# Kernel tuning notes

Hardware: AMD Instinct MI355X
Metric: run time of the kernel (lower is better)

The kernel has to match this reference:

```python
import jax, jax.numpy as jnp
import numpy as np
from jax import lax

B, C, OUT, K, L = 8, 256, 256, 7, 2048
STRIDE, PAD, DIL = 1, 3, 1

def setup_inputs() -> dict:
    key = jax.random.key(0)
    k1, k2, k3, k4, k5 = jax.random.split(key, 5)
    return {
        "x": jax.random.normal(k1, (B, C, L), jnp.float32),
        "w_off": jax.random.normal(k2, (C * K * 2, C, K), jnp.float32) * 0.02,
        "b_off": jax.random.normal(k3, (C * K * 2,), jnp.float32) * 0.02,
        "weight": jax.random.normal(k4, (OUT, C, K), jnp.float32) * 0.02,
        "bias": jax.random.normal(k5, (OUT,), jnp.float32) * 0.02,
    }

def _gather_lin(x, idx):
    # x: (B,C,Lin), idx: (B,C,K,Lout) -> zero-padded gather along length
    Lin = x.shape[-1]
    valid = (idx >= 0) & (idx < Lin)
    idxc = jnp.clip(idx, 0, Lin - 1)
    v = jnp.take_along_axis(x[:, :, None, :], idxc, axis=3)
    return jnp.where(valid, v, jnp.zeros((), x.dtype))

def reference(x, w_off, b_off, weight, bias):
    # offset/mask predictor conv (same geometry as main conv)
    off = lax.conv_general_dilated(
        x, w_off, window_strides=(STRIDE,), padding=[(PAD, PAD)],
        rhs_dilation=(DIL,), dimension_numbers=("NCH", "OIH", "NCH"))
    off = off + b_off[None, :, None]
    Lout = off.shape[-1]
    off = off.reshape(B, 2, C * K, Lout)
    offset = off[:, 0].reshape(B, C, K, Lout)          # fractional shift per (c,k,p)
    mask = jax.nn.sigmoid(off[:, 1]).reshape(B, C, K, Lout)
    # base sampling grid: p*stride - pad + k*dil
    base = (jnp.arange(Lout) * STRIDE - PAD)[None, :] + (jnp.arange(K) * DIL)[:, None]  # (K,Lout)
    pos = offset + base[None, None].astype(x.dtype)    # (B,C,K,Lout)
    p0 = jnp.floor(pos)
    frac = pos - p0
    p0i = p0.astype(jnp.int32)
    sampled = _gather_lin(x, p0i) * (1.0 - frac) + _gather_lin(x, p0i + 1) * frac
    sampled = sampled * mask
    # grouped conv accumulate (groups=1): (B,C,K,L) x (O,C,K) -> (B,O,L)
    out = jnp.einsum("bckl,ock->bol", sampled, weight) + bias[None, :, None]
    return out
```

## Files before the change

### kernel.cpp

```cpp
#include <hip/hip_runtime.h>

typedef unsigned short ushort_t;
typedef __attribute__((ext_vector_type(8))) short bf16x8;
typedef __attribute__((ext_vector_type(4))) float f32x4;

constexpr int BB   = 8;
constexpr int CC   = 256;
constexpr int OUTC = 256;
constexpr int KK   = 7;
constexpr int LL   = 2048;
constexpr int PADc = 3;
constexpr int KD   = CC * KK;
constexpr int MOFF = CC * KK * 2;
constexpr int NTOT = BB * LL;
constexpr int NKSTEPS = KD / 32;
constexpr int LP   = LL + 6;

__device__ __forceinline__ ushort_t f2bf(float f) {
    unsigned u = __float_as_uint(f);
    unsigned r = (u + 0x7fffu + ((u >> 16) & 1u)) >> 16;
    return (ushort_t)r;
}

__global__ __launch_bounds__(256) void cast_k(const float4* __restrict__ src,
                                              ushort_t* __restrict__ dst, int n4) {
    int i = blockIdx.x * 256 + threadIdx.x;
    if (i >= n4) return;
    float4 v = src[i];
    ushort4 o;
    o.x = f2bf(v.x); o.y = f2bf(v.y); o.z = f2bf(v.z); o.w = f2bf(v.w);
    *(ushort4*)(dst + (size_t)i * 4) = o;
}

__global__ __launch_bounds__(256) void castperm_woff(const float* __restrict__ src,
                                                     ushort_t* __restrict__ dst) {
    int i = blockIdx.x * 256 + threadIdx.x;
    if (i >= MOFF * KD) return;
    int dr  = i / KD;
    int rem = i - dr * KD;
    int kk = rem >> 8, c = rem & 255;
    int r = (dr & 1) ? (KD + (dr >> 1)) : (dr >> 1);
    dst[i] = f2bf(src[(r * 256 + c) * 7 + kk]);
}

__global__ __launch_bounds__(256) void xpose_k(const float* __restrict__ x,
                                               ushort_t* __restrict__ xp) {
    __shared__ float tile[32][257];
    int bid = blockIdx.x;
    int b  = bid >> 6;
    int l0 = ((bid >> 3) & 7) * 256;
    int c0 = (bid & 7) * 32;
    int tid = threadIdx.x;
    const float* xb = x + (size_t)b * (CC * LL);
    ushort_t* xpb = xp + (size_t)b * (LP * 256);
#pragma unroll 4
    for (int k = 0; k < 32; ++k)
        tile[k][tid] = xb[(size_t)(c0 + k) * LL + l0 + tid];
    __syncthreads();
    int lp = l0 + tid + 3;
#pragma unroll
    for (int q = 0; q < 8; ++q) {
        ushort4 v;
        v.x = f2bf(tile[4 * q + 0][tid]);
        v.y = f2bf(tile[4 * q + 1][tid]);
        v.z = f2bf(tile[4 * q + 2][tid]);
        v.w = f2bf(tile[4 * q + 3][tid]);
        *(ushort4*)(xpb + (size_t)lp * 256 + c0 + 4 * q) = v;
    }
    if ((bid & 63) == 0) {
#pragma unroll
        for (int r = 0; r < 6; ++r) {
            int glp = (r < 3) ? r : (2048 + r);
            xpb[glp * 256 + tid] = 0;
        }
    }
}

__device__ __forceinline__ void load_lds16(const ushort_t* g, ushort_t* l) {
    __builtin_amdgcn_global_load_lds(
        (const __attribute__((address_space(1))) unsigned int*)g,
        (__attribute__((address_space(3))) unsigned int*)l, 16, 0, 0);
}

__device__ __forceinline__ void stage256A(ushort_t* ldsbuf,
                                          const ushort_t* __restrict__ A,
                                          int m0, int kt, int wid, int lane) {
    int t = wid * 64 + lane;
    int g = (t & 3) ^ ((t >> 3) & 3);
#pragma unroll
    for (int j = 0; j < 2; ++j) {
        int row = j * 128 + (t >> 2);
        load_lds16(A + (size_t)(m0 + row) * KD + kt * 32 + g * 8,
                   ldsbuf + j * 4096 + wid * 512);
    }
}
__device__ __forceinline__ void stage256B(ushort_t* ldsbuf,
                                          const ushort_t* __restrict__ xp,
                                          int n0, int kt, int wid, int lane) {
    int t = wid * 64 + lane;
    int g = (t & 3) ^ ((t >> 3) & 3);
    int tap = kt >> 3, cs = kt & 7;
    const ushort_t* base = xp + (size_t)(n0 >> 11) * (LP * 256)
                              + (size_t)((n0 & 2047) + tap) * 256 + cs * 32 + g * 8;
#pragma unroll
    for (int j = 0; j < 2; ++j) {
        int row = j * 128 + (t >> 2);
        load_lds16(base + (size_t)row * 256,
                   ldsbuf + 8192 + j * 4096 + wid * 512);
    }
}

template <int VMC>
__device__ __forceinline__ void kstep256(const ushort_t* __restrict__ A,
                                         const ushort_t* __restrict__ xp,
                                         ushort_t* lds, int m0, int n0, int kt,
                                         int wid, int lane, int wr, int wc,
                                         int r15, int u, f32x4 (&acc)[8][4]) {
    asm volatile("s_waitcnt vmcnt(%0)" :: "n"(VMC) : "memory");
    __builtin_amdgcn_s_barrier();
    const ushort_t* buf = lds + (size_t)(kt & 3) * 16384;
    const ushort_t* pa = buf + (wr * 128 + r15) * 32 + u * 8;
    const ushort_t* pb = buf + 8192 + (wc * 64 + r15) * 32 + u * 8;
    bf16x8 af[8], bq[4];
#pragma unroll
    for (int i = 0; i < 8; ++i) af[i] = *(const bf16x8*)(pa + i * 512);
#pragma unroll
    for (int j = 0; j < 4; ++j) bq[j] = *(const bf16x8*)(pb + j * 512);
    if (kt + 3 < NKSTEPS) {
        stage256A(lds + (size_t)((kt + 3) & 3) * 16384, A,  m0, kt + 3, wid, lane);
        stage256B(lds + (size_t)((kt + 3) & 3) * 16384, xp, n0, kt + 3, wid, lane);
    }
    __builtin_amdgcn_s_setprio(1);
#pragma unroll
    for (int i = 0; i < 8; ++i)
#pragma unroll
        for (int j = 0; j < 4; ++j)
            acc[i][j] = __builtin_amdgcn_mfma_f32_16x16x32_bf16(af[i], bq[j], acc[i][j], 0, 0, 0);
    __builtin_amdgcn_s_setprio(0);
}

__global__ __launch_bounds__(512, 2) void gemm256_off_fused(const ushort_t* __restrict__ A,
                                                            const ushort_t* __restrict__ xp,
                                                            const float* __restrict__ boff,
                                                            const float* __restrict__ x,
                                                            ushort_t* __restrict__ s) {
    __shared__ __align__(16) ushort_t lds[4 * 16384];
    constexpr int NT = NTOT / 256;
    constexpr int NWG = (MOFF / 256) * NT;
    int bid = blockIdx.x;
    int wg = (bid & 7) * (NWG / 8) + (bid >> 3);
    int mt = wg / NT, nt = wg % NT;
    int m0 = mt * 256, n0 = nt * 256;
    int tid = threadIdx.x, wid = tid >> 6, lane = tid & 63;
    int wr = wid >> 2, wc = wid & 3;
    int r15 = lane & 15, kh = lane >> 4;
    int u = kh ^ ((r15 >> 1) & 3);

    f32x4 acc[8][4] = {};

    stage256A(lds,             A,  m0, 0, wid, lane);
    stage256B(lds,             xp, n0, 0, wid, lane);
    stage256A(lds + 16384,     A,  m0, 1, wid, lane);
    stage256B(lds + 16384,     xp, n0, 1, wid, lane);
    stage256A(lds + 2 * 16384, A,  m0, 2, wid, lane);
    stage256B(lds + 2 * 16384, xp, n0, 2, wid, lane);

    for (int kt = 0; kt < NKSTEPS - 2; ++kt)
        kstep256<8>(A, xp, lds, m0, n0, kt, wid, lane, wr, wc, r15, u, acc);
    kstep256<4>(A, xp, lds, m0, n0, NKSTEPS - 2, wid, lane, wr, wc, r15, u, acc);
    kstep256<0>(A, xp, lds, m0, n0, NKSTEPS - 1, wid, lane, wr, wc, r15, u, acc);

    __syncthreads();
    ushort_t* st = lds;
#pragma unroll
    for (int i = 0; i < 8; ++i) {
        int mloc = wr * 128 + i * 16 + kh * 4;
        int ckb  = (m0 + mloc) >> 1;
        int ckl  = mloc >> 1;
        float bo0 = boff[ckb],     bm0 = boff[KD + ckb];
        float bo1 = boff[ckb + 1], bm1 = boff[KD + ckb + 1];
        int c0 = ckb / 7,       kk0 = ckb - c0 * 7;
        int c1 = (ckb + 1) / 7, kk1 = (ckb + 1) - c1 * 7;
#pragma unroll
        for (int j = 0; j < 4; ++j) {
            int nl = wc * 64 + j * 16 + r15;
            int n = n0 + nl;
            int b = n >> 11, l = n & 2047;
            const float* xb_ = x + (size_t)b * (CC * LL);
            f32x4 v = acc[i][j];
            ushort2 o2;
#pragma unroll
            for (int p = 0; p < 2; ++p) {
                float offv = v[2 * p]     + (p ? bo1 : bo0);
                float mpre = v[2 * p + 1] + (p ? bm1 : bm0);
                int c = p ? c1 : c0, kk = p ? kk1 : kk0;
                float mask = 1.0f / (1.0f + __expf(-mpre));
                float pos = offv + (float)(l - PADc + kk);
                float p0f = floorf(pos);
                float frac = pos - p0f;
                int p0 = (int)p0f;
                const float* xr = xb_ + (size_t)c * LL;
                float x0 = ((unsigned)p0 < (unsigned)LL) ? xr[p0] : 0.0f;
                float x1 = ((unsigned)(p0 + 1) < (unsigned)LL) ? xr[p0 + 1] : 0.0f;
                float sv = (x0 + (x1 - x0) * frac) * mask;
                if (p) o2.y = f2bf(sv); else o2.x = f2bf(sv);
            }
            *(ushort2*)(st + nl * 136 + ckl) = o2;
        }
    }
    __syncthreads();
    int srow = tid >> 5, scol = tid & 31;
    int ck0g = m0 >> 1;
#pragma unroll
    for (int pass = 0; pass < 16; ++pass) {
        int nl = pass * 16 + srow;
        ushort4 v4 = *(const ushort4*)(st + nl * 136 + scol * 4);
        *(ushort4*)(s + (size_t)(n0 + nl) * KD + ck0g + scol * 4) = v4;
    }
}

__device__ __forceinline__ void stage128(ushort_t* ldsbuf,
                                         const ushort_t* __restrict__ A,
                                         const ushort_t* __restrict__ Bt,
                                         int m0, int n0, int kt,
                                         int wid, int lane) {
    int t = wid * 64 + lane;
    int g = (t & 3) ^ ((t >> 3) & 3);
#pragma unroll
    for (int j = 0; j < 2; ++j) {
        int row = j * 64 + (t >> 2);
        load_lds16(A  + (size_t)(m0 + row) * KD + kt * 32 + g * 8,
                   ldsbuf + j * 2048 + wid * 512);
        load_lds16(Bt + (size_t)(n0 + row) * KD + kt * 32 + g * 8,
                   ldsbuf + 4096 + j * 2048 + wid * 512);
    }
}

template <int VMC>
__device__ __forceinline__ void kstep128(const ushort_t* __restrict__ A,
                                         const ushort_t* __restrict__ Bt,
                                         ushort_t* lds, int m0, int n0, int kt,
                                         int wid, int lane, int wr, int wc,
                                         int r15, int u, f32x4 (&acc)[4][4]) {
    asm volatile("s_waitcnt vmcnt(%0)" :: "n"(VMC) : "memory");
    __builtin_amdgcn_s_barrier();
    const ushort_t* buf = lds + (size_t)(kt & 3) * 8192;
    const ushort_t* pa = buf + (wr * 64 + r15) * 32 + u * 8;
    const ushort_t* pb = buf + 4096 + (wc * 64 + r15) * 32 + u * 8;
    bf16x8 af[4], bq[4];
#pragma unroll
    for (int i = 0; i < 4; ++i) af[i] = *(const bf16x8*)(pa + i * 512);
#pragma unroll
    for (int j = 0; j < 4; ++j) bq[j] = *(const bf16x8*)(pb + j * 512);
    if (kt + 3 < NKSTEPS)
        stage128(lds + (size_t)((kt + 3) & 3) * 8192, A, Bt, m0, n0, kt + 3, wid, lane);
    __builtin_amdgcn_s_setprio(1);
#pragma unroll
    for (int i = 0; i < 4; ++i)
#pragma unroll
        for (int j = 0; j < 4; ++j)
            acc[i][j] = __builtin_amdgcn_mfma_f32_16x16x32_bf16(af[i], bq[j], acc[i][j], 0, 0, 0);
    __builtin_amdgcn_s_setprio(0);
}

__global__ __launch_bounds__(256, 2) void gemm128_out(const ushort_t* __restrict__ A,
                                                      const ushort_t* __restrict__ Bt,
                                                      const float* __restrict__ bvec,
                                                      float* __restrict__ Dout) {
    __shared__ __align__(16) ushort_t lds[4 * 8192];
    constexpr int NT = NTOT / 128;
    constexpr int NWG = (OUTC / 128) * NT;
    int bid = blockIdx.x;
    int wg = (bid & 7) * (NWG / 8) + (bid >> 3);
    int mt = wg / NT, nt = wg % NT;
    int m0 = mt * 128, n0 = nt * 128;
    int tid = threadIdx.x, wid = tid >> 6, lane = tid & 63;
    int wr = wid >> 1, wc = wid & 1;
    int r15 = lane & 15, kh = lane >> 4;
    int u = kh ^ ((r15 >> 1) & 3);

    f32x4 acc[4][4] = {};

    stage128(lds,            A, Bt, m0, n0, 0, wid, lane);
    stage128(lds + 8192,     A, Bt, m0, n0, 1, wid, lane);
    stage128(lds + 2 * 8192, A, Bt, m0, n0, 2, wid, lane);

    for (int kt = 0; kt < NKSTEPS - 2; ++kt)
        kstep128<8>(A, Bt, lds, m0, n0, kt, wid, lane, wr, wc, r15, u, acc);
    kstep128<4>(A, Bt, lds, m0, n0, NKSTEPS - 2, wid, lane, wr, wc, r15, u, acc);
    kstep128<0>(A, Bt, lds, m0, n0, NKSTEPS - 1, wid, lane, wr, wc, r15, u, acc);

    int rbase = kh * 4;
#pragma unroll
    for (int i = 0; i < 4; ++i)
#pragma unroll
        for (int j = 0; j < 4; ++j) {
            int m = m0 + wr * 64 + i * 16 + rbase;
            int n = n0 + wc * 64 + j * 16 + r15;
            int b = n >> 11, l = n & 2047;
#pragma unroll
            for (int r = 0; r < 4; ++r) {
                float val = acc[i][j][r] + bvec[m + r];
                Dout[((size_t)(b * OUTC + (m + r))) * LL + l] = val;
            }
        }
}

extern "C" void kernel_launch(void* const* d_in, const int* in_sizes, int n_in,
                              void* d_out, int out_size, void* d_ws, size_t ws_size,
                              hipStream_t stream) {
    const float* x      = (const float*)d_in[0];
    const float* w_off  = (const float*)d_in[1];
    const float* b_off  = (const float*)d_in[2];
    const float* weight = (const float*)d_in[3];
    const float* bias   = (const float*)d_in[4];
    float* out = (float*)d_out;

    ushort_t* w = (ushort_t*)d_ws;
    ushort_t* wb  = w;
    ushort_t* wtb = wb  + MOFF * KD;
    ushort_t* xp  = wtb + OUTC * KD;
    ushort_t* s   = xp  + BB * LP * 256;

    castperm_woff<<<(MOFF * KD + 255) / 256, 256, 0, stream>>>(w_off, wb);
    cast_k<<<(114688 + 255) / 256, 256, 0, stream>>>((const float4*)weight, wtb, 114688);
    xpose_k<<<512, 256, 0, stream>>>(x, xp);

    gemm256_off_fused<<<(MOFF / 256) * (NTOT / 256), 512, 0, stream>>>(wb, xp, b_off, x, s);

    gemm128_out<<<(OUTC / 128) * (NTOT / 128), 256, 0, stream>>>(wtb, s, bias, out);
}
```

Measured before the change: 307.0 us.

## Shrink offset GEMM tile to 128x256 with triple-buffered LDS for occupancy

Changes the fused offset-conv GEMM tile from 256x256 to 128x256 (M halved). The LDS ring goes from four 256x256 buffers with three steps of prefetch to three smaller buffers with two steps of prefetch. Launch bounds rise to 4 blocks per CU and the grid doubles, aiming for more resident waves and better latency hiding. The epilogue staging stride and write-out are reshaped to 16-byte stores. The trade-off is lower per-tile reuse: each B tile is loaded twice as often across M, and prefetch depth is shallower.

Result: no change. 308.8 us (+0.6%).

```diff
diff --git a/kernel.cpp b/kernel.cpp
--- a/kernel.cpp
+++ b/kernel.cpp
@@ -3,6 +3,7 @@
 typedef unsigned short ushort_t;
 typedef __attribute__((ext_vector_type(8))) short bf16x8;
 typedef __attribute__((ext_vector_type(4))) float f32x4;
+typedef __attribute__((ext_vector_type(8))) unsigned short ushort8;
 
 constexpr int BB   = 8;
 constexpr int CC   = 256;
@@ -15,6 +16,7 @@
 constexpr int NTOT = BB * LL;
 constexpr int NKSTEPS = KD / 32;
 constexpr int LP   = LL + 6;
+constexpr int BUFU = 12288;
 
 __device__ __forceinline__ ushort_t f2bf(float f) {
     unsigned u = __float_as_uint(f);
@@ -82,99 +84,93 @@
         (__attribute__((address_space(3))) unsigned int*)l, 16, 0, 0);
 }
 
-__device__ __forceinline__ void stage256A(ushort_t* ldsbuf,
+__device__ __forceinline__ void stageA128(ushort_t* ldsbuf,
                                           const ushort_t* __restrict__ A,
-                                          int m0, int kt, int wid, int lane) {
-    int t = wid * 64 + lane;
-    int g = (t & 3) ^ ((t >> 3) & 3);
-#pragma unroll
-    for (int j = 0; j < 2; ++j) {
-        int row = j * 128 + (t >> 2);
-        load_lds16(A + (size_t)(m0 + row) * KD + kt * 32 + g * 8,
-                   ldsbuf + j * 4096 + wid * 512);
-    }
-}
-__device__ __forceinline__ void stage256B(ushort_t* ldsbuf,
+                                          int m0, int kt, int tid) {
+    int g = (tid & 3) ^ ((tid >> 3) & 3);
+    int row = tid >> 2;
+    load_lds16(A + (size_t)(m0 + row) * KD + kt * 32 + g * 8,
+               ldsbuf + (tid >> 6) * 512);
+}
+__device__ __forceinline__ void stageB256(ushort_t* ldsbuf,
                                           const ushort_t* __restrict__ xp,
-                                          int n0, int kt, int wid, int lane) {
-    int t = wid * 64 + lane;
-    int g = (t & 3) ^ ((t >> 3) & 3);
+                                          int n0, int kt, int tid) {
+    int g = (tid & 3) ^ ((tid >> 3) & 3);
     int tap = kt >> 3, cs = kt & 7;
     const ushort_t* base = xp + (size_t)(n0 >> 11) * (LP * 256)
                               + (size_t)((n0 & 2047) + tap) * 256 + cs * 32 + g * 8;
 #pragma unroll
     for (int j = 0; j < 2; ++j) {
-        int row = j * 128 + (t >> 2);
+        int row = j * 128 + (tid >> 2);
         load_lds16(base + (size_t)row * 256,
-                   ldsbuf + 8192 + j * 4096 + wid * 512);
-    }
-}
-
-template <int VMC>
-__device__ __forceinline__ void kstep256(const ushort_t* __restrict__ A,
-                                         const ushort_t* __restrict__ xp,
-                                         ushort_t* lds, int m0, int n0, int kt,
-                                         int wid, int lane, int wr, int wc,
-                                         int r15, int u, f32x4 (&acc)[8][4]) {
+                   ldsbuf + 4096 + j * 4096 + (tid >> 6) * 512);
+    }
+}
+
+template <int VMC, bool PF>
+__device__ __forceinline__ void kstepN(const ushort_t* __restrict__ A,
+                                       const ushort_t* __restrict__ xp,
+                                       ushort_t* lds, int m0, int n0, int kt,
+                                       int tid, int wr, int wc,
+                                       int r15, int u, f32x4 (&acc)[4][4]) {
     asm volatile("s_waitcnt vmcnt(%0)" :: "n"(VMC) : "memory");
     __builtin_amdgcn_s_barrier();
-    const ushort_t* buf = lds + (size_t)(kt & 3) * 16384;
-    const ushort_t* pa = buf + (wr * 128 + r15) * 32 + u * 8;
-    const ushort_t* pb = buf + 8192 + (wc * 64 + r15) * 32 + u * 8;
-    bf16x8 af[8], bq[4];
-#pragma unroll
-    for (int i = 0; i < 8; ++i) af[i] = *(const bf16x8*)(pa + i * 512);
+    const ushort_t* buf = lds + (size_t)(kt % 3) * BUFU;
+    const ushort_t* pa = buf + (wr * 64 + r15) * 32 + u * 8;
+    const ushort_t* pb = buf + 4096 + (wc * 64 + r15) * 32 + u * 8;
+    bf16x8 af[4], bq[4];
+#pragma unroll
+    for (int i = 0; i < 4; ++i) af[i] = *(const bf16x8*)(pa + i * 512);
 #pragma unroll
     for (int j = 0; j < 4; ++j) bq[j] = *(const bf16x8*)(pb + j * 512);
-    if (kt + 3 < NKSTEPS) {
-        stage256A(lds + (size_t)((kt + 3) & 3) * 16384, A,  m0, kt + 3, wid, lane);
-        stage256B(lds + (size_t)((kt + 3) & 3) * 16384, xp, n0, kt + 3, wid, lane);
+    if (PF) {
+        ushort_t* nb = lds + (size_t)((kt + 2) % 3) * BUFU;
+        stageA128(nb, A,  m0, kt + 2, tid);
+        stageB256(nb, xp, n0, kt + 2, tid);
     }
     __builtin_amdgcn_s_setprio(1);
 #pragma unroll
-    for (int i = 0; i < 8; ++i)
+    for (int i = 0; i < 4; ++i)
 #pragma unroll
         for (int j = 0; j < 4; ++j)
             acc[i][j] = __builtin_amdgcn_mfma_f32_16x16x32_bf16(af[i], bq[j], acc[i][j], 0, 0, 0);
     __builtin_amdgcn_s_setprio(0);
 }
 
-__global__ __launch_bounds__(512, 2) void gemm256_off_fused(const ushort_t* __restrict__ A,
-                                                            const ushort_t* __restrict__ xp,
-                                                            const float* __restrict__ boff,
-                                                            const float* __restrict__ x,
-                                                            ushort_t* __restrict__ s) {
-    __shared__ __align__(16) ushort_t lds[4 * 16384];
+__global__ __launch_bounds__(512, 4) void gemm128n_off_fused(const ushort_t* __restrict__ A,
+                                                             const ushort_t* __restrict__ xp,
+                                                             const float* __restrict__ boff,
+                                                             const float* __restrict__ x,
+                                                             ushort_t* __restrict__ s) {
+    __shared__ __align__(16) ushort_t lds[3 * BUFU];
     constexpr int NT = NTOT / 256;
-    constexpr int NWG = (MOFF / 256) * NT;
+    constexpr int NWG = (MOFF / 128) * NT;
     int bid = blockIdx.x;
     int wg = (bid & 7) * (NWG / 8) + (bid >> 3);
     int mt = wg / NT, nt = wg % NT;
-    int m0 = mt * 256, n0 = nt * 256;
+    int m0 = mt * 128, n0 = nt * 256;
     int tid = threadIdx.x, wid = tid >> 6, lane = tid & 63;
     int wr = wid >> 2, wc = wid & 3;
     int r15 = lane & 15, kh = lane >> 4;
     int u = kh ^ ((r15 >> 1) & 3);
 
-    f32x4 acc[8][4] = {};
-
-    stage256A(lds,             A,  m0, 0, wid, lane);
-    stage256B(lds,             xp, n0, 0, wid, lane);
-    stage256A(lds + 16384,     A,  m0, 1, wid, lane);
-    stage256B(lds + 16384,     xp, n0, 1, wid, lane);
-    stage256A(lds + 2 * 16384, A,  m0, 2, wid, lane);
-    stage256B(lds + 2 * 16384, xp, n0, 2, wid, lane);
+    f32x4 acc[4][4] = {};
+
+    stageA128(lds,        A,  m0, 0, tid);
+    stageB256(lds,        xp, n0, 0, tid);
+    stageA128(lds + BUFU, A,  m0, 1, tid);
+    stageB256(lds + BUFU, xp, n0, 1, tid);
 
     for (int kt = 0; kt < NKSTEPS - 2; ++kt)
-        kstep256<8>(A, xp, lds, m0, n0, kt, wid, lane, wr, wc, r15, u, acc);
-    kstep256<4>(A, xp, lds, m0, n0, NKSTEPS - 2, wid, lane, wr, wc, r15, u, acc);
-    kstep256<0>(A, xp, lds, m0, n0, NKSTEPS - 1, wid, lane, wr, wc, r15, u, acc);
+        kstepN<3, true>(A, xp, lds, m0, n0, kt, tid, wr, wc, r15, u, acc);
+    kstepN<3, false>(A, xp, lds, m0, n0, NKSTEPS - 2, tid, wr, wc, r15, u, acc);
+    kstepN<0, false>(A, xp, lds, m0, n0, NKSTEPS - 1, tid, wr, wc, r15, u, acc);
 
     __syncthreads();
     ushort_t* st = lds;
 #pragma unroll
-    for (int i = 0; i < 8; ++i) {
-        int mloc = wr * 128 + i * 16 + kh * 4;
+    for (int i = 0; i < 4; ++i) {
+        int mloc = wr * 64 + i * 16 + kh * 4;
         int ckb  = (m0 + mloc) >> 1;
         int ckl  = mloc >> 1;
         float bo0 = boff[ckb],     bm0 = boff[KD + ckb];
@@ -205,17 +201,18 @@
                 float sv = (x0 + (x1 - x0) * frac) * mask;
                 if (p) o2.y = f2bf(sv); else o2.x = f2bf(sv);
             }
-            *(ushort2*)(st + nl * 136 + ckl) = o2;
+            *(ushort2*)(st + nl * 72 + ckl) = o2;
         }
     }
     __syncthreads();
-    int srow = tid >> 5, scol = tid & 31;
+    int srow = tid >> 3;
+    int scol = tid & 7;
     int ck0g = m0 >> 1;
 #pragma unroll
-    for (int pass = 0; pass < 16; ++pass) {
-        int nl = pass * 16 + srow;
-        ushort4 v4 = *(const ushort4*)(st + nl * 136 + scol * 4);
-        *(ushort4*)(s + (size_t)(n0 + nl) * KD + ck0g + scol * 4) = v4;
+    for (int pass = 0; pass < 4; ++pass) {
+        int nl = pass * 64 + srow;
+        ushort8 v8 = *(const ushort8*)(st + nl * 72 + scol * 8);
+        *(ushort8*)(s + (size_t)(n0 + nl) * KD + ck0g + scol * 8) = v8;
     }
 }
 
@@ -326,7 +323,7 @@
     cast_k<<<(114688 + 255) / 256, 256, 0, stream>>>((const float4*)weight, wtb, 114688);
     xpose_k<<<512, 256, 0, stream>>>(x, xp);
 
-    gemm256_off_fused<<<(MOFF / 256) * (NTOT / 256), 512, 0, stream>>>(wb, xp, b_off, x, s);
+    gemm128n_off_fused<<<(MOFF / 128) * (NTOT / 256), 512, 0, stream>>>(wb, xp, b_off, x, s);
 
     gemm128_out<<<(OUTC / 128) * (NTOT / 128), 256, 0, stream>>>(wtb, s, bias, out);
 }
```

## Restructure offset GEMM into ping-pong double-buffered 64-deep K pipeline

Applied to the files above, without the earlier changes.

Rewrites the offset-predictor GEMM main loop to use 64-wide K tiles, split into half-tiles, with two LDS buffers. Global-to-LDS staging is interleaved between quarter-sized MFMA groups, separated by barriers, in a ping-pong schedule. The w_off permutation is changed to match the new K ordering (channel-slice-major, then tap), and the LDS swizzle is widened to 8 groups. Launch bounds drop to one block per CU, which gives up occupancy in exchange for explicit overlap of loads with MFMA work. The many added barriers add synchronisation cost.

New measurement: 286.7 us. 6.6% less time.

```diff
diff --git a/kernel.cpp b/kernel.cpp
--- a/kernel.cpp
+++ b/kernel.cpp
@@ -3,6 +3,7 @@
 typedef unsigned short ushort_t;
 typedef __attribute__((ext_vector_type(8))) short bf16x8;
 typedef __attribute__((ext_vector_type(4))) float f32x4;
+typedef __attribute__((ext_vector_type(8))) unsigned short ushort8;
 
 constexpr int BB   = 8;
 constexpr int CC   = 256;
@@ -14,6 +15,8 @@
 constexpr int MOFF = CC * KK * 2;
 constexpr int NTOT = BB * LL;
 constexpr int NKSTEPS = KD / 32;
+constexpr int NT64 = KD / 64;
+constexpr int NITER = NT64 / 2;
 constexpr int LP   = LL + 6;
 
 __device__ __forceinline__ ushort_t f2bf(float f) {
@@ -37,10 +40,14 @@
     int i = blockIdx.x * 256 + threadIdx.x;
     if (i >= MOFF * KD) return;
     int dr  = i / KD;
-    int rem = i - dr * KD;
-    int kk = rem >> 8, c = rem & 255;
+    int q   = i - dr * KD;
+    int cs   = q / 224;
+    int r224 = q - cs * 224;
+    int tap  = r224 >> 5;
+    int cl   = r224 & 31;
+    int c = cs * 32 + cl;
     int r = (dr & 1) ? (KD + (dr >> 1)) : (dr >> 1);
-    dst[i] = f2bf(src[(r * 256 + c) * 7 + kk]);
+    dst[i] = f2bf(src[(r * 256 + c) * 7 + tap]);
 }
 
 __global__ __launch_bounds__(256) void xpose_k(const float* __restrict__ x,
@@ -82,69 +89,134 @@
         (__attribute__((address_space(3))) unsigned int*)l, 16, 0, 0);
 }
 
-__device__ __forceinline__ void stage256A(ushort_t* ldsbuf,
-                                          const ushort_t* __restrict__ A,
-                                          int m0, int kt, int wid, int lane) {
-    int t = wid * 64 + lane;
-    int g = (t & 3) ^ ((t >> 3) & 3);
+__device__ __forceinline__ void stageA8(ushort_t* dsthalf, const ushort_t* __restrict__ A,
+                                        int m0, int h, int tile, int wid, int lane) {
+    int gs = (lane & 7) ^ ((lane >> 3) & 7);
 #pragma unroll
     for (int j = 0; j < 2; ++j) {
-        int row = j * 128 + (t >> 2);
-        load_lds16(A + (size_t)(m0 + row) * KD + kt * 32 + g * 8,
-                   ldsbuf + j * 4096 + wid * 512);
-    }
-}
-__device__ __forceinline__ void stage256B(ushort_t* ldsbuf,
-                                          const ushort_t* __restrict__ xp,
-                                          int n0, int kt, int wid, int lane) {
-    int t = wid * 64 + lane;
-    int g = (t & 3) ^ ((t >> 3) & 3);
-    int tap = kt >> 3, cs = kt & 7;
+        int rl = (wid * 2 + j) * 8 + (lane >> 3);
+        load_lds16(A + (size_t)(m0 + h * 128 + rl) * KD + tile * 64 + gs * 8,
+                   dsthalf + (wid * 2 + j) * 512);
+    }
+}
+__device__ __forceinline__ void stageB8(ushort_t* dsthalf, const ushort_t* __restrict__ xp,
+                                        int n0, int h, int tile, int wid, int lane) {
+    int gs = (lane & 7) ^ ((lane >> 3) & 7);
+    int ks = tile * 2 + (gs >> 2);
+    int cs = ks / 7, tap = ks - cs * 7;
     const ushort_t* base = xp + (size_t)(n0 >> 11) * (LP * 256)
-                              + (size_t)((n0 & 2047) + tap) * 256 + cs * 32 + g * 8;
+                         + (size_t)((n0 & 2047) + h * 128 + tap) * 256 + cs * 32 + (gs & 3) * 8;
 #pragma unroll
     for (int j = 0; j < 2; ++j) {
-        int row = j * 128 + (t >> 2);
-        load_lds16(base + (size_t)row * 256,
-                   ldsbuf + 8192 + j * 4096 + wid * 512);
-    }
-}
-
-template <int VMC>
-__device__ __forceinline__ void kstep256(const ushort_t* __restrict__ A,
-                                         const ushort_t* __restrict__ xp,
-                                         ushort_t* lds, int m0, int n0, int kt,
-                                         int wid, int lane, int wr, int wc,
-                                         int r15, int u, f32x4 (&acc)[8][4]) {
-    asm volatile("s_waitcnt vmcnt(%0)" :: "n"(VMC) : "memory");
-    __builtin_amdgcn_s_barrier();
-    const ushort_t* buf = lds + (size_t)(kt & 3) * 16384;
-    const ushort_t* pa = buf + (wr * 128 + r15) * 32 + u * 8;
-    const ushort_t* pb = buf + 8192 + (wc * 64 + r15) * 32 + u * 8;
-    bf16x8 af[8], bq[4];
-#pragma unroll
-    for (int i = 0; i < 8; ++i) af[i] = *(const bf16x8*)(pa + i * 512);
-#pragma unroll
-    for (int j = 0; j < 4; ++j) bq[j] = *(const bf16x8*)(pb + j * 512);
-    if (kt + 3 < NKSTEPS) {
-        stage256A(lds + (size_t)((kt + 3) & 3) * 16384, A,  m0, kt + 3, wid, lane);
-        stage256B(lds + (size_t)((kt + 3) & 3) * 16384, xp, n0, kt + 3, wid, lane);
-    }
+        int rl = (wid * 2 + j) * 8 + (lane >> 3);
+        load_lds16(base + (size_t)rl * 256, dsthalf + (wid * 2 + j) * 512);
+    }
+}
+
+__device__ __forceinline__ void rdA(bf16x8 (&af)[4][2], const ushort_t* dA,
+                                    int rbase, int r15, int kh) {
+#pragma unroll
+    for (int f = 0; f < 4; ++f)
+#pragma unroll
+        for (int q = 0; q < 2; ++q) {
+            int row = rbase + f * 16 + r15;
+            af[f][q] = *(const bf16x8*)(dA + row * 64 + ((q * 4 + kh) ^ (r15 & 7)) * 8);
+        }
+}
+__device__ __forceinline__ void rdB(bf16x8 (&bq)[4][2], int c0f, const ushort_t* dB,
+                                    int cbase, int r15, int kh) {
+#pragma unroll
+    for (int f = 0; f < 2; ++f)
+#pragma unroll
+        for (int q = 0; q < 2; ++q) {
+            int row = cbase + f * 16 + r15;
+            bq[c0f + f][q] = *(const bf16x8*)(dB + row * 64 + ((q * 4 + kh) ^ (r15 & 7)) * 8);
+        }
+}
+
+template <int I0, int J0>
+__device__ __forceinline__ void mfmaQ(f32x4 (&acc)[8][4], const bf16x8 (&af)[4][2],
+                                      const bf16x8 (&bq)[4][2]) {
     __builtin_amdgcn_s_setprio(1);
 #pragma unroll
-    for (int i = 0; i < 8; ++i)
-#pragma unroll
-        for (int j = 0; j < 4; ++j)
-            acc[i][j] = __builtin_amdgcn_mfma_f32_16x16x32_bf16(af[i], bq[j], acc[i][j], 0, 0, 0);
+    for (int i = 0; i < 4; ++i)
+#pragma unroll
+        for (int j = 0; j < 2; ++j)
+#pragma unroll
+            for (int q = 0; q < 2; ++q)
+                acc[I0 + i][J0 + j] = __builtin_amdgcn_mfma_f32_16x16x32_bf16(
+                    af[i][q], bq[J0 + j][q], acc[I0 + i][J0 + j], 0, 0, 0);
     __builtin_amdgcn_s_setprio(0);
 }
 
-__global__ __launch_bounds__(512, 2) void gemm256_off_fused(const ushort_t* __restrict__ A,
-                                                            const ushort_t* __restrict__ xp,
-                                                            const float* __restrict__ boff,
-                                                            const float* __restrict__ x,
-                                                            ushort_t* __restrict__ s) {
-    __shared__ __align__(16) ushort_t lds[4 * 16384];
+#define BAR()   __builtin_amdgcn_s_barrier()
+#define LGKM0() asm volatile("s_waitcnt lgkmcnt(0)" ::: "memory")
+#define VMC(n)  asm volatile("s_waitcnt vmcnt(%0)" :: "n"(n) : "memory")
+
+template <int MODE>
+__device__ __forceinline__ void iter8(const ushort_t* __restrict__ A,
+                                      const ushort_t* __restrict__ xp,
+                                      ushort_t* lds, int m0, int n0, int it,
+                                      int wid, int lane, int wr, int wc, int r15, int kh,
+                                      f32x4 (&acc)[8][4]) {
+    const int t1 = 2 * it + 1, t2 = 2 * it + 2, t3 = 2 * it + 3;
+    const ushort_t* d0A = lds;
+    const ushort_t* d0B = lds + 16384;
+    const ushort_t* d1A = lds + 32768;
+    const ushort_t* d1B = lds + 49152;
+    ushort_t* w0A = lds;         ushort_t* w0B = lds + 16384;
+    ushort_t* w1A = lds + 32768; ushort_t* w1B = lds + 49152;
+    bf16x8 af[4][2], bq[4][2];
+
+    rdA(af, d0A, wr * 128, r15, kh);
+    rdB(bq, 0, d0B, wc * 64, r15, kh);
+    stageB8(w1B + 8192, xp, n0, 1, t1, wid, lane);
+    BAR(); LGKM0();
+    mfmaQ<0, 0>(acc, af, bq);
+    BAR();
+    rdB(bq, 2, d0B, wc * 64 + 32, r15, kh);
+    stageA8(w1A + 8192, A, m0, 1, t1, wid, lane);
+    BAR(); LGKM0();
+    mfmaQ<0, 2>(acc, af, bq);
+    BAR();
+    rdA(af, d0A, wr * 128 + 64, r15, kh);
+    if (MODE == 0) stageB8(w0B, xp, n0, 0, t2, wid, lane);
+    BAR(); LGKM0();
+    mfmaQ<4, 0>(acc, af, bq);
+    BAR();
+    if (MODE == 0) { stageA8(w0A, A, m0, 0, t2, wid, lane); VMC(4); }
+    else           { VMC(0); }
+    BAR();
+    mfmaQ<4, 2>(acc, af, bq);
+    BAR();
+    rdA(af, d1A, wr * 128, r15, kh);
+    rdB(bq, 0, d1B, wc * 64, r15, kh);
+    if (MODE == 0) stageB8(w0B + 8192, xp, n0, 1, t2, wid, lane);
+    BAR(); LGKM0();
+    mfmaQ<0, 0>(acc, af, bq);
+    BAR();
+    rdB(bq, 2, d1B, wc * 64 + 32, r15, kh);
+    if (MODE == 0) stageA8(w0A + 8192, A, m0, 1, t2, wid, lane);
+    BAR(); LGKM0();
+    mfmaQ<0, 2>(acc, af, bq);
+    BAR();
+    rdA(af, d1A, wr * 128 + 64, r15, kh);
+    if (MODE == 0) stageB8(w1B, xp, n0, 0, t3, wid, lane);
+    BAR(); LGKM0();
+    mfmaQ<4, 0>(acc, af, bq);
+    BAR();
+    if (MODE == 0) { stageA8(w1A, A, m0, 0, t3, wid, lane); VMC(4); }
+    BAR();
+    mfmaQ<4, 2>(acc, af, bq);
+    BAR();
+}
+
+__global__ __launch_bounds__(512, 1) void gemm256p_off_fused(const ushort_t* __restrict__ A,
+                                                             const ushort_t* __restrict__ xp,
+                                                             const float* __restrict__ boff,
+                                                             const float* __restrict__ x,
+                                                             ushort_t* __restrict__ s) {
+    __shared__ __align__(16) ushort_t lds[65536];
     constexpr int NT = NTOT / 256;
     constexpr int NWG = (MOFF / 256) * NT;
     int bid = blockIdx.x;
@@ -154,21 +226,22 @@
     int tid = threadIdx.x, wid = tid >> 6, lane = tid & 63;
     int wr = wid >> 2, wc = wid & 3;
     int r15 = lane & 15, kh = lane >> 4;
-    int u = kh ^ ((r15 >> 1) & 3);
 
     f32x4 acc[8][4] = {};
 
-    stage256A(lds,             A,  m0, 0, wid, lane);
-    stage256B(lds,             xp, n0, 0, wid, lane);
-    stage256A(lds + 16384,     A,  m0, 1, wid, lane);
-    stage256B(lds + 16384,     xp, n0, 1, wid, lane);
-    stage256A(lds + 2 * 16384, A,  m0, 2, wid, lane);
-    stage256B(lds + 2 * 16384, xp, n0, 2, wid, lane);
-
-    for (int kt = 0; kt < NKSTEPS - 2; ++kt)
-        kstep256<8>(A, xp, lds, m0, n0, kt, wid, lane, wr, wc, r15, u, acc);
-    kstep256<4>(A, xp, lds, m0, n0, NKSTEPS - 2, wid, lane, wr, wc, r15, u, acc);
-    kstep256<0>(A, xp, lds, m0, n0, NKSTEPS - 1, wid, lane, wr, wc, r15, u, acc);
+    stageB8(lds + 16384,         xp, n0, 0, 0, wid, lane);
+    stageA8(lds,                 A,  m0, 0, 0, wid, lane);
+    stageB8(lds + 16384 + 8192,  xp, n0, 1, 0, wid, lane);
+    stageA8(lds + 8192,          A,  m0, 1, 0, wid, lane);
+    stageB8(lds + 49152,         xp, n0, 0, 1, wid, lane);
+    stageA8(lds + 32768,         A,  m0, 0, 1, wid, lane);
+    VMC(4);
+    BAR();
+
+#pragma unroll 1
+    for (int it = 0; it < NITER - 1; ++it)
+        iter8<0>(A, xp, lds, m0, n0, it, wid, lane, wr, wc, r15, kh, acc);
+    iter8<1>(A, xp, lds, m0, n0, NITER - 1, wid, lane, wr, wc, r15, kh, acc);
 
     __syncthreads();
     ushort_t* st = lds;
@@ -236,13 +309,13 @@
     }
 }
 
-template <int VMC>
+template <int VMCN>
 __device__ __forceinline__ void kstep128(const ushort_t* __restrict__ A,
                                          const ushort_t* __restrict__ Bt,
                                          ushort_t* lds, int m0, int n0, int kt,
                                          int wid, int lane, int wr, int wc,
                                          int r15, int u, f32x4 (&acc)[4][4]) {
-    asm volatile("s_waitcnt vmcnt(%0)" :: "n"(VMC) : "memory");
+    asm volatile("s_waitcnt vmcnt(%0)" :: "n"(VMCN) : "memory");
     __builtin_amdgcn_s_barrier();
     const ushort_t* buf = lds + (size_t)(kt & 3) * 8192;
     const ushort_t* pa = buf + (wr * 64 + r15) * 32 + u * 8;
@@ -326,7 +399,7 @@
     cast_k<<<(114688 + 255) / 256, 256, 0, stream>>>((const float4*)weight, wtb, 114688);
     xpose_k<<<512, 256, 0, stream>>>(x, xp);
 
-    gemm256_off_fused<<<(MOFF / 256) * (NTOT / 256), 512, 0, stream>>>(wb, xp, b_off, x, s);
+    gemm256p_off_fused<<<(MOFF / 256) * (NTOT / 256), 512, 0, stream>>>(wb, xp, b_off, x, s);
 
     gemm128_out<<<(OUTC / 128) * (NTOT / 128), 256, 0, stream>>>(wtb, s, bias, out);
 }
```
